# Kernel optimization log

Measured on AMD Instinct MI355X. Metric: run time of the kernel, lower is better.

The kernel has to match this reference:

```python
import jax, jax.numpy as jnp
import numpy as np

DIM = 2048; S = 2048; B = 2; H = 16
Q_LORA = 1536; KV_LORA = 512
NOPE = 128; ROPE = 64; VHD = 128
QK_HD = NOPE + ROPE  # 192


def _linear_params(key, out_dim, in_dim):
    k1, k2 = jax.random.split(key)
    w = jax.random.normal(k1, (out_dim, in_dim), jnp.float32) * 0.02
    b = jax.random.normal(k2, (out_dim,), jnp.float32) * 0.02
    return w, b


def setup_inputs() -> dict:
    key = jax.random.key(0)
    ks = jax.random.split(key, 8)
    x = jax.random.normal(ks[0], (B, S, DIM), jnp.float32)
    # RoPE tables (interleaved convention, half-dim = ROPE//2)
    inv_freq = 1.0 / (10000.0 ** (jnp.arange(ROPE // 2, dtype=jnp.float32) / (ROPE // 2)))
    ang = jnp.arange(S, dtype=jnp.float32)[:, None] * inv_freq[None, :]  # [S, 32]
    freqs_cos = jnp.cos(ang)
    freqs_sin = jnp.sin(ang)
    Wq_down_w, Wq_down_b = _linear_params(ks[1], Q_LORA, DIM)
    q_norm_w = jnp.ones((Q_LORA,), jnp.float32)
    Wq_up_w, Wq_up_b = _linear_params(ks[2], H * QK_HD, Q_LORA)
    Wkv_down_w, Wkv_down_b = _linear_params(ks[3], KV_LORA + ROPE, DIM)
    kv_norm_w = jnp.ones((KV_LORA,), jnp.float32)
    Wkv_up_w, Wkv_up_b = _linear_params(ks[4], H * (NOPE + VHD), KV_LORA)
    Wo_w, Wo_b = _linear_params(ks[5], DIM, H * VHD)
    return dict(x=x, freqs_cos=freqs_cos, freqs_sin=freqs_sin,
                Wq_down_w=Wq_down_w, Wq_down_b=Wq_down_b, q_norm_w=q_norm_w,
                Wq_up_w=Wq_up_w, Wq_up_b=Wq_up_b,
                Wkv_down_w=Wkv_down_w, Wkv_down_b=Wkv_down_b, kv_norm_w=kv_norm_w,
                Wkv_up_w=Wkv_up_w, Wkv_up_b=Wkv_up_b, Wo_w=Wo_w, Wo_b=Wo_b)


def _rmsnorm(x, w):
    eps = jnp.finfo(x.dtype).eps
    var = jnp.mean(jnp.square(x), axis=-1, keepdims=True)
    return x * jax.lax.rsqrt(var + eps) * w


def _rope(x, cos, sin):
    # x: [B, S, H, D] with consecutive (real, imag) pairs; cos/sin: [S, D//2]
    xr = x[..., 0::2]
    xi = x[..., 1::2]
    c = cos[None, :, None, :]
    s = sin[None, :, None, :]
    yr = xr * c - xi * s
    yi = xr * s + xi * c
    return jnp.stack([yr, yi], axis=-1).reshape(x.shape)


def reference(x, freqs_cos, freqs_sin, Wq_down_w, Wq_down_b, q_norm_w,
              Wq_up_w, Wq_up_b, Wkv_down_w, Wkv_down_b, kv_norm_w,
              Wkv_up_w, Wkv_up_b, Wo_w, Wo_b):
    Bx, Sx, _ = x.shape
    # Q path: down-proj -> RMSNorm -> up-proj
    q_lat = _rmsnorm(x @ Wq_down_w.T + Wq_down_b, q_norm_w)
    Q = (q_lat @ Wq_up_w.T + Wq_up_b).reshape(Bx, Sx, H, QK_HD)
    Q_nope, Q_rope = Q[..., :NOPE], Q[..., NOPE:]
    Q_rope = _rope(Q_rope, freqs_cos, freqs_sin)
    Q = jnp.concatenate([Q_nope, Q_rope], axis=-1)
    # KV path
    kv = x @ Wkv_down_w.T + Wkv_down_b
    kv_lat, k_rope = kv[..., :KV_LORA], kv[..., KV_LORA:]
    kv_lat = _rmsnorm(kv_lat, kv_norm_w)
    k_rope = _rope(k_rope[:, :, None, :], freqs_cos, freqs_sin)  # [B,S,1,ROPE]
    knv = (kv_lat @ Wkv_up_w.T + Wkv_up_b).reshape(Bx, Sx, H, NOPE + VHD)
    K_nope, V = knv[..., :NOPE], knv[..., NOPE:]
    K = jnp.concatenate([K_nope, jnp.broadcast_to(k_rope, (Bx, Sx, H, ROPE))], axis=-1)
    # causal SDPA, scale = 1/sqrt(qk_head_dim)
    scale = QK_HD ** -0.5
    scores = jnp.einsum('bqhd,bkhd->bhqk', Q, K) * scale
    causal = jnp.tril(jnp.ones((Sx, Sx), bool))
    scores = jnp.where(causal[None, None], scores, jnp.finfo(scores.dtype).min)
    attn = jax.nn.softmax(scores, axis=-1)
    out = jnp.einsum('bhqk,bkhd->bqhd', attn, V).reshape(Bx, Sx, H * VHD)
    return out @ Wo_w.T + Wo_b
```

## Files before the change

### kernel.cpp

```cpp
#include <hip/hip_runtime.h>
#include <hip/hip_bf16.h>

typedef unsigned short u16;
typedef short s16x8 __attribute__((ext_vector_type(8)));
typedef short s16x4 __attribute__((ext_vector_type(4)));
typedef float f32x4 __attribute__((ext_vector_type(4)));

#define SEQ   2048
#define BATCH 2
#define NHEAD 16

__device__ __forceinline__ float b2f(u16 u) {
    unsigned x = ((unsigned)u) << 16;
    return __builtin_bit_cast(float, x);
}
__device__ __forceinline__ u16 f2b(float f) {
    unsigned x = __builtin_bit_cast(unsigned, f);
    unsigned r = (x + 0x7fffu + ((x >> 16) & 1u)) >> 16;
    return (u16)r;
}
__device__ __forceinline__ u16 f2b_hw(float f) {
    return __builtin_bit_cast(u16, __float2bfloat16(f));
}
__device__ __forceinline__ s16x8 comb(s16x4 lo, s16x4 hi) {
    return __builtin_shufflevector(lo, hi, 0, 1, 2, 3, 4, 5, 6, 7);
}
__device__ __forceinline__ void gload16(const void* g, void* l) {
    __builtin_amdgcn_global_load_lds(
        (const __attribute__((address_space(1))) void*)g,
        (__attribute__((address_space(3))) void*)l, 16, 0, 0);
}

__global__ __launch_bounds__(256) void cvt4_k(
    const float* __restrict__ x, const float* __restrict__ wqd,
    const float* __restrict__ wkvd, const float* __restrict__ wqu,
    u16* __restrict__ xb, u16* __restrict__ wqdb,
    u16* __restrict__ wkvdb, u16* __restrict__ wqub)
{
    const int total = 4358144;
    int i = blockIdx.x * 256 + threadIdx.x;
    const int stride = gridDim.x * 256;
    for (; i < total; i += stride) {
        const float4* src; ushort4* dst; int off;
        if (i < 2097152)      { src = (const float4*)x;    dst = (ushort4*)xb;    off = i; }
        else if (i < 2883584) { src = (const float4*)wqd;  dst = (ushort4*)wqdb;  off = i - 2097152; }
        else if (i < 3178496) { src = (const float4*)wkvd; dst = (ushort4*)wkvdb; off = i - 2883584; }
        else                  { src = (const float4*)wqu;  dst = (ushort4*)wqub;  off = i - 3178496; }
        float4 v = src[off];
        ushort4 o = { f2b(v.x), f2b(v.y), f2b(v.z), f2b(v.w) };
        dst[off] = o;
    }
}

__global__ __launch_bounds__(256) void cvt_bf16_k(
    const float* __restrict__ in, u16* __restrict__ out, int n4)
{
    int i = blockIdx.x * 256 + threadIdx.x;
    const int stride = gridDim.x * 256;
    for (; i < n4; i += stride) {
        float4 v = ((const float4*)in)[i];
        ushort4 o = { f2b(v.x), f2b(v.y), f2b(v.z), f2b(v.w) };
        ((ushort4*)out)[i] = o;
    }
}

template <int MODE, int TM>
__global__ __launch_bounds__(512, 2) void gemm8p_k(
    const u16* __restrict__ A, const u16* __restrict__ W0,
    const u16* __restrict__ W1, const float* __restrict__ b0,
    const float* __restrict__ b1, void* __restrict__ C0, void* __restrict__ C1,
    int N, int K, int lda,
    const float* __restrict__ fc, const float* __restrict__ fs)
{
    constexpr int AH  = TM / 128;
    constexpr int MPP = TM == 256 ? 2 : 1;
    __shared__ u16 lsA[2][AH][128 * 64];
    __shared__ u16 lsB[2][2][128 * 64];
    const int tid  = threadIdx.x;
    const int lane = tid & 63;
    const int w    = tid >> 6;
    const int wm   = w >> 2;
    const int wn   = w & 3;
    const int row0 = blockIdx.y * TM;
    const int col0 = blockIdx.x * 256;
    const int nt   = K / 64;

    auto stageA = [&](int t, int h) {
        const int kt = t * 64, buf = t & 1;
#pragma unroll
        for (int j = 0; j < 2; j++) {
            const int g = (w * 2 + j) * 64 + lane;
            const int row = g >> 3, c16 = g & 7;
            const int cs = c16 ^ (row & 7);
            gload16(A + (size_t)(row0 + h * 128 + row) * lda + kt + cs * 8,
                    &lsA[buf][h][(w * 2 + j) * 512]);
        }
    };
    auto stageB = [&](int t, int h) {
        const int kt = t * 64, buf = t & 1;
#pragma unroll
        for (int j = 0; j < 2; j++) {
            const int g = (w * 2 + j) * 64 + lane;
            const int row = g >> 3, c16 = g & 7;
            const int cs = c16 ^ (row & 7);
            int rw = col0 + h * 128 + row;
            const u16* Wp;
            if (MODE == 3) {
                const bool in1 = rw >= 1536;
                int r2 = in1 ? rw - 1536 : rw;
                if (in1 && r2 > 575) r2 = 575;
                Wp = (in1 ? W1 : W0) + (size_t)r2 * K;
            } else {
                if (rw >= N) rw = N - 1;
                Wp = W0 + (size_t)rw * K;
            }
            gload16(Wp + kt + cs * 8, &lsB[buf][h][(w * 2 + j) * 512]);
        }
    };
    auto readA = [&](int buf, int mf, int kh) -> s16x8 {
        const int h  = TM == 256 ? wm : 0;
        const int ra = (TM == 256 ? mf * 16 : wm * 64 + mf * 16) + (lane & 15);
        const int c16 = kh * 4 + (lane >> 4);
        return *(const s16x8*)&lsA[buf][h][(ra * 8 + (c16 ^ (ra & 7))) * 8];
    };
    auto readB = [&](int buf, int nf, int kh) -> s16x8 {
        const int rb = (wn & 1) * 64 + nf * 16 + (lane & 15);
        const int c16 = kh * 4 + (lane >> 4);
        return *(const s16x8*)&lsB[buf][wn >> 1][(rb * 8 + (c16 ^ (rb & 7))) * 8];
    };

    f32x4 acc[4 * MPP][4];
#pragma unroll
    for (int i = 0; i < 4 * MPP; i++)
#pragma unroll
        for (int j = 0; j < 4; j++) acc[i][j] = (f32x4){0.f, 0.f, 0.f, 0.f};

    stageB(0, 0); stageB(0, 1);
#pragma unroll
    for (int h = 0; h < AH; h++) stageA(0, h);
    stageB(1, 0); stageB(1, 1);
    asm volatile("s_waitcnt vmcnt(4)" ::: "memory");
    asm volatile("s_barrier" ::: "memory");

    for (int t = 0; t < nt; t++) {
        const int buf = t & 1;
        s16x8 bfr[4][2];
#pragma unroll
        for (int nf = 0; nf < 4; nf++)
#pragma unroll
            for (int kh = 0; kh < 2; kh++) bfr[nf][kh] = readB(buf, nf, kh);
#pragma unroll
        for (int ph = 0; ph < 4; ph++) {
            s16x8 af[MPP][2];
#pragma unroll
            for (int m2 = 0; m2 < MPP; m2++)
#pragma unroll
                for (int kh = 0; kh < 2; kh++)
                    af[m2][kh] = readA(buf, ph * MPP + m2, kh);
            if (ph == 0) { if (t + 1 < nt) stageA(t + 1, 0); }
            else if (ph == 1) {
                if (TM == 256) { if (t + 1 < nt) stageA(t + 1, 1); }
                if (t + 2 < nt) stageB(t + 2, 0);
            } else if (ph == 2) { if (t + 2 < nt) stageB(t + 2, 1); }
            __builtin_amdgcn_s_setprio(1);
#pragma unroll
            for (int kh = 0; kh < 2; kh++)
#pragma unroll
                for (int m2 = 0; m2 < MPP; m2++)
#pragma unroll
                    for (int nf = 0; nf < 4; nf++)
                        acc[ph * MPP + m2][nf] = __builtin_amdgcn_mfma_f32_16x16x32_bf16(
                            af[m2][kh], bfr[nf][kh], acc[ph * MPP + m2][nf], 0, 0, 0);
            __builtin_amdgcn_s_setprio(0);
            if (ph == 0) asm volatile("s_barrier" ::: "memory");
        }
        if (t + 2 < nt) asm volatile("s_waitcnt vmcnt(4)" ::: "memory");
        else            asm volatile("s_waitcnt vmcnt(0)" ::: "memory");
        asm volatile("s_barrier" ::: "memory");
    }

    const float QS = 0.10411754f;
    const int rbase = row0 + wm * (TM == 256 ? 128 : 64) + ((lane >> 4) << 2);
    const int cbase = col0 + wn * 64 + (lane & 15);
#pragma unroll
    for (int nf = 0; nf < 4; nf++) {
        const int col = cbase + nf * 16;
        if (MODE == 3) {
            if (col < 2112) {
                const bool c1 = col >= 1536;
                const float bv = c1 ? b1[col - 1536] : b0[col];
#pragma unroll
                for (int mf = 0; mf < 4 * MPP; mf++)
#pragma unroll
                    for (int r = 0; r < 4; r++) {
                        const int row = rbase + mf * 16 + r;
                        const float v = acc[mf][nf][r] + bv;
                        if (c1) ((u16*)C1)[(size_t)row * 576 + col - 1536] = f2b_hw(v);
                        else    ((u16*)C0)[(size_t)row * 1536 + col] = f2b_hw(v);
                    }
            }
        } else if (MODE == 2) {
            const float bv = b0[col];
            const int colBase = col0 + wn * 64 + nf * 16;
            const int dh0 = colBase % 192;
            const bool ropeBlk = (dh0 >= 128);
            const int ib = (dh0 - 128 + (lane & 15)) >> 1;
#pragma unroll
            for (int mf = 0; mf < 4 * MPP; mf++)
#pragma unroll
                for (int r = 0; r < 4; r++) {
                    const int row = rbase + mf * 16 + r;
                    float v = acc[mf][nf][r] + bv;
                    if (ropeBlk) {
                        const float pp = __shfl_xor(v, 1);
                        const int s = row & (SEQ - 1);
                        const float c = fc[s * 32 + ib], sn = fs[s * 32 + ib];
                        v = (lane & 1) ? (v * c + pp * sn) : (v * c - pp * sn);
                    }
                    ((u16*)C0)[(size_t)row * 3072 + col] = f2b_hw(v * QS);
                }
        } else {
            if (col < N) {
                const float bv = b0[col];
#pragma unroll
                for (int mf = 0; mf < 4 * MPP; mf++)
#pragma unroll
                    for (int r = 0; r < 4; r++) {
                        const int row = rbase + mf * 16 + r;
                        const float v = acc[mf][nf][r] + bv;
                        if (MODE == 1) ((float*)C0)[(size_t)row * N + col] = v;
                        else           ((u16*)C0)[(size_t)row * N + col] = f2b_hw(v);
                    }
            }
        }
    }
}

__global__ __launch_bounds__(256) void norm_rope_k(
    u16* __restrict__ qlat, u16* __restrict__ kvb,
    const float* __restrict__ qnw, const float* __restrict__ kvnw,
    const float* __restrict__ fc, const float* __restrict__ fs,
    u16* __restrict__ krope)
{
    const int bid = blockIdx.x;
    const int row = bid & 4095;
    const bool isq = bid < 4096;
    u16* xr = isq ? qlat + (size_t)row * 1536 : kvb + (size_t)row * 576;
    const int cols = isq ? 1536 : 512;
    const float* wv = isq ? qnw : kvnw;

    if (!isq && threadIdx.x < 32) {
        const int i = threadIdx.x;
        const int s = row & (SEQ - 1);
        const u16* src = kvb + (size_t)row * 576 + 512 + 2 * i;
        const float xr0 = b2f(src[0]), xi0 = b2f(src[1]);
        const float c = fc[s * 32 + i], sn = fs[s * 32 + i];
        ushort2 o;
        o.x = f2b(xr0 * c - xi0 * sn);
        o.y = f2b(xr0 * sn + xi0 * c);
        *((ushort2*)(krope + (size_t)row * 64) + i) = o;
    }

    float ss = 0.f;
    for (int c = threadIdx.x; c < cols; c += 256) { float v = b2f(xr[c]); ss += v * v; }
#pragma unroll
    for (int off = 32; off; off >>= 1) ss += __shfl_xor(ss, off);
    __shared__ float red[4];
    if ((threadIdx.x & 63) == 0) red[threadIdx.x >> 6] = ss;
    __syncthreads();
    const float tot = red[0] + red[1] + red[2] + red[3];
    const float inv = rsqrtf(tot / (float)cols + 1.1920929e-7f);
    for (int c = threadIdx.x; c < cols; c += 256)
        xr[c] = f2b(b2f(xr[c]) * inv * wv[c]);
}

__global__ __launch_bounds__(256, 2) void attn_k(
    const u16* __restrict__ Q, const u16* __restrict__ KNV,
    const u16* __restrict__ KR, u16* __restrict__ O)
{
    __shared__ u16 k_lds[64][204];
    __shared__ u16 v_t[128][76];

    const int tid  = threadIdx.x;
    const int lane = tid & 63;
    const int w    = tid >> 6;
    const int lr   = lane & 15;
    const int lq   = lane >> 4;

    const int bid = blockIdx.x;
    const int qt  = (bid < 256) ? (15 - (bid >> 5)) : ((bid - 256) >> 5);
    const int bh  = bid & 31;
    const int h   = bh & 15;
    const int b   = bh >> 4;
    const int q0  = qt * 128;
    const int bS  = b * SEQ;

    s16x8 qf[2][6];
#pragma unroll
    for (int mb = 0; mb < 2; mb++) {
        const u16* qp = Q + (size_t)(bS + q0 + w * 32 + mb * 16 + lr) * 3072
                        + h * 192 + (lq << 2);
#pragma unroll
        for (int kc = 0; kc < 6; kc++)
            qf[mb][kc] = comb(*(const s16x4*)(qp + kc * 32),
                              *(const s16x4*)(qp + kc * 32 + 16));
    }

    f32x4 o_acc[2][8];
#pragma unroll
    for (int mb = 0; mb < 2; mb++)
#pragma unroll
        for (int d = 0; d < 8; d++) o_acc[mb][d] = (f32x4){0.f, 0.f, 0.f, 0.f};
    float m_run[2] = { -1e30f, -1e30f };
    float l_run[2] = { 0.f, 0.f };

    const int ntiles = (q0 + 128) / 64;
    const int qmax_w = q0 + w * 32 + 31;

    s16x8 kr[6], vr[4];
    const int kkey = tid >> 2;
    const int ka   = tid & 3;

    {
        const u16* kn  = KNV + (size_t)(bS + kkey) * 4096 + h * 256;
        const u16* krp = KR + (size_t)(bS + kkey) * 64;
#pragma unroll
        for (int i = 0; i < 6; i++) {
            const int col = ka * 48 + i * 8;
            kr[i] = *(const s16x8*)(col < 128 ? kn + col : krp + (col - 128));
        }
#pragma unroll
        for (int i = 0; i < 4; i++) {
            const int idx = tid + i * 256;
            vr[i] = *(const s16x8*)(KNV + (size_t)(bS + (idx >> 4)) * 4096
                                    + h * 256 + 128 + (idx & 15) * 8);
        }
    }

    for (int t = 0; t < ntiles; t++) {
#pragma unroll
        for (int i = 0; i < 6; i++) {
            const int c0 = ka * 48 + i * 8;
            *(s16x4*)&k_lds[kkey][c0]     = __builtin_shufflevector(kr[i], kr[i], 0, 1, 2, 3);
            *(s16x4*)&k_lds[kkey][c0 + 4] = __builtin_shufflevector(kr[i], kr[i], 4, 5, 6, 7);
        }
#pragma unroll
        for (int i = 0; i < 4; i++) {
            const int idx = tid + i * 256;
            const int key = idx >> 4, d0 = (idx & 15) * 8;
            const int xw = (d0 >> 4) << 2;
#pragma unroll
            for (int e = 0; e < 8; e++) v_t[d0 + e][key ^ xw] = (u16)vr[i][e];
        }
        __syncthreads();

        if (t + 1 < ntiles) {
            const int nk = (t + 1) * 64;
            const u16* kn  = KNV + (size_t)(bS + nk + kkey) * 4096 + h * 256;
            const u16* krp = KR + (size_t)(bS + nk + kkey) * 64;
#pragma unroll
            for (int i = 0; i < 6; i++) {
                const int col = ka * 48 + i * 8;
                kr[i] = *(const s16x8*)(col < 128 ? kn + col : krp + (col - 128));
            }
#pragma unroll
            for (int i = 0; i < 4; i++) {
                const int idx = tid + i * 256;
                vr[i] = *(const s16x8*)(KNV + (size_t)(bS + nk + (idx >> 4)) * 4096
                                        + h * 256 + 128 + (idx & 15) * 8);
            }
        }

        const int kt0 = t * 64;
        if (kt0 <= qmax_w) {
            f32x4 sa[2][4];
#pragma unroll
            for (int mb = 0; mb < 2; mb++)
#pragma unroll
                for (int f = 0; f < 4; f++) sa[mb][f] = (f32x4){0.f, 0.f, 0.f, 0.f};
#pragma unroll
            for (int kc = 0; kc < 6; kc++) {
                const int kb = kc * 32 + (lq << 2);
#pragma unroll
                for (int f = 0; f < 4; f++) {
                    s16x8 kf = comb(*(const s16x4*)&k_lds[f * 16 + lr][kb],
                                    *(const s16x4*)&k_lds[f * 16 + lr][kb + 16]);
                    sa[0][f] = __builtin_amdgcn_mfma_f32_16x16x32_bf16(kf, qf[0][kc], sa[0][f], 0, 0, 0);
                    sa[1][f] = __builtin_amdgcn_mfma_f32_16x16x32_bf16(kf, qf[1][kc], sa[1][f], 0, 0, 0);
                }
            }

            s16x8 pb[2][2];
#pragma unroll
            for (int mb = 0; mb < 2; mb++) {
                const int qrow = q0 + w * 32 + mb * 16 + lr;
                const bool need_mask = (kt0 + 63 > qrow);
                float p[4][4];
#pragma unroll
                for (int f = 0; f < 4; f++)
#pragma unroll
                    for (int r = 0; r < 4; r++) {
                        float s = sa[mb][f][r];
                        if (need_mask && (kt0 + f * 16 + lq * 4 + r > qrow)) s = -1e30f;
                        p[f][r] = s;
                    }
                float tm = p[0][0];
#pragma unroll
                for (int f = 0; f < 4; f++)
#pragma unroll
                    for (int r = 0; r < 4; r++) tm = fmaxf(tm, p[f][r]);
                tm = fmaxf(tm, __shfl_xor(tm, 16));
                tm = fmaxf(tm, __shfl_xor(tm, 32));

                const float mo = m_run[mb];
                const bool keep = __all(tm <= mo + 8.f);
                float corr = 1.f;
                if (!keep) {
                    const float nm = fmaxf(mo, tm);
                    corr = __builtin_amdgcn_exp2f(mo - nm);
                    m_run[mb] = nm;
                }
                const float mbase = m_run[mb];
#pragma unroll
                for (int f = 0; f < 4; f++)
#pragma unroll
                    for (int r = 0; r < 4; r++)
                        p[f][r] = __builtin_amdgcn_exp2f(p[f][r] - mbase);
                float ps = 0.f;
#pragma unroll
                for (int f = 0; f < 4; f++)
#pragma unroll
                    for (int r = 0; r < 4; r++) ps += p[f][r];
                ps += __shfl_xor(ps, 16);
                ps += __shfl_xor(ps, 32);
                l_run[mb] = l_run[mb] * corr + ps;
                if (!keep) {
#pragma unroll
                    for (int d = 0; d < 8; d++)
#pragma unroll
                        for (int r = 0; r < 4; r++) o_acc[mb][d][r] *= corr;
                }
#pragma unroll
                for (int hf = 0; hf < 2; hf++) {
                    s16x8 v;
#pragma unroll
                    for (int j = 0; j < 8; j++)
                        v[j] = (short)f2b_hw(p[hf * 2 + (j >> 2)][j & 3]);
                    pb[mb][hf] = v;
                }
            }

#pragma unroll
            for (int hf = 0; hf < 2; hf++) {
                const int pc = hf * 32 + (lq << 2);
#pragma unroll
                for (int df = 0; df < 8; df++) {
                    const int row = df * 16 + lr;
                    const int xr0 = df << 2;
                    s16x8 vf = comb(*(const s16x4*)&v_t[row][pc ^ xr0],
                                    *(const s16x4*)&v_t[row][(pc + 16) ^ xr0]);
                    o_acc[0][df] = __builtin_amdgcn_mfma_f32_16x16x32_bf16(vf, pb[0][hf], o_acc[0][df], 0, 0, 0);
                    o_acc[1][df] = __builtin_amdgcn_mfma_f32_16x16x32_bf16(vf, pb[1][hf], o_acc[1][df], 0, 0, 0);
                }
            }
        }
        __syncthreads();
    }

#pragma unroll
    for (int mb = 0; mb < 2; mb++) {
        const float invl = 1.f / l_run[mb];
        u16* op = O + (size_t)(bS + q0 + w * 32 + mb * 16 + lr) * 2048 + h * 128 + lq * 4;
#pragma unroll
        for (int df = 0; df < 8; df++) {
            ushort4 ov = { f2b_hw(o_acc[mb][df][0] * invl), f2b_hw(o_acc[mb][df][1] * invl),
                           f2b_hw(o_acc[mb][df][2] * invl), f2b_hw(o_acc[mb][df][3] * invl) };
            *(ushort4*)(op + df * 16) = ov;
        }
    }
}

extern "C" void kernel_launch(void* const* d_in, const int* in_sizes, int n_in,
                              void* d_out, int out_size, void* d_ws, size_t ws_size,
                              hipStream_t stream)
{
    const float* x    = (const float*)d_in[0];
    const float* fc   = (const float*)d_in[1];
    const float* fs   = (const float*)d_in[2];
    const float* Wqd  = (const float*)d_in[3];
    const float* bqd  = (const float*)d_in[4];
    const float* qnw  = (const float*)d_in[5];
    const float* Wqu  = (const float*)d_in[6];
    const float* bqu  = (const float*)d_in[7];
    const float* Wkvd = (const float*)d_in[8];
    const float* bkvd = (const float*)d_in[9];
    const float* kvnw = (const float*)d_in[10];
    const float* Wkvu = (const float*)d_in[11];
    const float* bkvu = (const float*)d_in[12];
    const float* Wo   = (const float*)d_in[13];
    const float* bo   = (const float*)d_in[14];

    char* ws = (char*)d_ws;
    u16* kvb     = (u16*)(ws);
    u16* qlat    = (u16*)(ws + 4718592);
    u16* qbuf    = (u16*)(ws + 17301504);
    u16* krope   = (u16*)(ws + 42467328);
    u16* knv     = (u16*)(ws + 42991616);
    u16* attn_o  = (u16*)(ws);
    u16* x_bf    = (u16*)(ws + 17301504);
    u16* wqd_bf  = (u16*)(ws + 42991616);
    u16* wkvd_bf = (u16*)(ws + 49283072);
    u16* wqu_bf  = (u16*)(ws + 51642368);
    u16* wkvu_bf = (u16*)(ws + 4718592);
    u16* wo_bf   = (u16*)(ws + 42991616);

    cvt4_k<<<2048, 256, 0, stream>>>(x, Wqd, Wkvd, Wqu, x_bf, wqd_bf, wkvd_bf, wqu_bf);
    gemm8p_k<3, 256><<<dim3(9, 16), 512, 0, stream>>>(
        x_bf, wqd_bf, wkvd_bf, bqd, bkvd, qlat, kvb, 2112, 2048, 2048, nullptr, nullptr);
    norm_rope_k<<<8192, 256, 0, stream>>>(qlat, kvb, qnw, kvnw, fc, fs, krope);
    gemm8p_k<2, 256><<<dim3(12, 16), 512, 0, stream>>>(
        qlat, wqu_bf, nullptr, bqu, nullptr, qbuf, nullptr, 3072, 1536, 1536, fc, fs);
    cvt_bf16_k<<<1024, 256, 0, stream>>>(Wkvu, wkvu_bf, 2097152 / 4);
    gemm8p_k<0, 256><<<dim3(16, 16), 512, 0, stream>>>(
        kvb, wkvu_bf, nullptr, bkvu, nullptr, knv, nullptr, 4096, 512, 576, nullptr, nullptr);
    attn_k<<<512, 256, 0, stream>>>(qbuf, knv, krope, attn_o);
    cvt_bf16_k<<<1024, 256, 0, stream>>>(Wo, wo_bf, 4194304 / 4);
    gemm8p_k<1, 128><<<dim3(8, 32), 512, 0, stream>>>(
        attn_o, wo_bf, nullptr, bo, nullptr, d_out, nullptr, 2048, 2048, 2048, nullptr, nullptr);
}
```

Baseline: 345.5 us.

## Fuse fp32-to-bf16 conversion of x into the down-projection GEMM A-load

Drops the standalone conversion of x to bf16. The first GEMM now loads fp32 x rows into registers, converts them, and writes them to LDS at a later phase, replacing the async global-to-LDS copy. This removes a full write and re-read of the bf16 copy of x. In exchange, GEMM register pressure rises and each iteration waits on an extra LDS count. Separately, the norm kernel is vectorised to 8-element loads and stores, with the row kept in registers between reduction and scaling.

```diff
diff --git a/kernel.cpp b/kernel.cpp
--- a/kernel.cpp
+++ b/kernel.cpp
@@ -31,21 +31,19 @@
         (__attribute__((address_space(3))) void*)l, 16, 0, 0);
 }
 
-__global__ __launch_bounds__(256) void cvt4_k(
-    const float* __restrict__ x, const float* __restrict__ wqd,
-    const float* __restrict__ wkvd, const float* __restrict__ wqu,
-    u16* __restrict__ xb, u16* __restrict__ wqdb,
-    u16* __restrict__ wkvdb, u16* __restrict__ wqub)
+__global__ __launch_bounds__(256) void cvt3_k(
+    const float* __restrict__ wqd, const float* __restrict__ wkvd,
+    const float* __restrict__ wqu,
+    u16* __restrict__ wqdb, u16* __restrict__ wkvdb, u16* __restrict__ wqub)
 {
-    const int total = 4358144;
+    const int total = 2260992;
     int i = blockIdx.x * 256 + threadIdx.x;
     const int stride = gridDim.x * 256;
     for (; i < total; i += stride) {
         const float4* src; ushort4* dst; int off;
-        if (i < 2097152)      { src = (const float4*)x;    dst = (ushort4*)xb;    off = i; }
-        else if (i < 2883584) { src = (const float4*)wqd;  dst = (ushort4*)wqdb;  off = i - 2097152; }
-        else if (i < 3178496) { src = (const float4*)wkvd; dst = (ushort4*)wkvdb; off = i - 2883584; }
-        else                  { src = (const float4*)wqu;  dst = (ushort4*)wqub;  off = i - 3178496; }
+        if (i < 786432)       { src = (const float4*)wqd;  dst = (ushort4*)wqdb;  off = i; }
+        else if (i < 1081344) { src = (const float4*)wkvd; dst = (ushort4*)wkvdb; off = i - 786432; }
+        else                  { src = (const float4*)wqu;  dst = (ushort4*)wqub;  off = i - 1081344; }
         float4 v = src[off];
         ushort4 o = { f2b(v.x), f2b(v.y), f2b(v.z), f2b(v.w) };
         dst[off] = o;
@@ -66,7 +64,7 @@
 
 template <int MODE, int TM>
 __global__ __launch_bounds__(512, 2) void gemm8p_k(
-    const u16* __restrict__ A, const u16* __restrict__ W0,
+    const void* __restrict__ Av, const u16* __restrict__ W0,
     const u16* __restrict__ W1, const float* __restrict__ b0,
     const float* __restrict__ b1, void* __restrict__ C0, void* __restrict__ C1,
     int N, int K, int lda,
@@ -74,6 +72,7 @@
 {
     constexpr int AH  = TM / 128;
     constexpr int MPP = TM == 256 ? 2 : 1;
+    constexpr bool AF32 = (MODE == 3);
     __shared__ u16 lsA[2][AH][128 * 64];
     __shared__ u16 lsB[2][2][128 * 64];
     const int tid  = threadIdx.x;
@@ -85,6 +84,8 @@
     const int col0 = blockIdx.x * 256;
     const int nt   = K / 64;
 
+    float4 afl[AH][2][2];
+
     auto stageA = [&](int t, int h) {
         const int kt = t * 64, buf = t & 1;
 #pragma unroll
@@ -92,8 +93,31 @@
             const int g = (w * 2 + j) * 64 + lane;
             const int row = g >> 3, c16 = g & 7;
             const int cs = c16 ^ (row & 7);
-            gload16(A + (size_t)(row0 + h * 128 + row) * lda + kt + cs * 8,
+            gload16((const u16*)Av + (size_t)(row0 + h * 128 + row) * lda + kt + cs * 8,
                     &lsA[buf][h][(w * 2 + j) * 512]);
+        }
+    };
+    auto issueAf32 = [&](int t, int h) {
+        const float* X = (const float*)Av;
+        const int kt = t * 64;
+#pragma unroll
+        for (int j = 0; j < 2; j++) {
+            const int g = (w * 2 + j) * 64 + lane;
+            const int row = g >> 3, c16 = g & 7;
+            const int cs = c16 ^ (row & 7);
+            const float* p = X + (size_t)(row0 + h * 128 + row) * lda + kt + cs * 8;
+            afl[h][j][0] = *(const float4*)p;
+            afl[h][j][1] = *(const float4*)(p + 4);
+        }
+    };
+    auto writeAf32 = [&](int t, int h) {
+        const int buf = t & 1;
+#pragma unroll
+        for (int j = 0; j < 2; j++) {
+            const float4 lo = afl[h][j][0], hi = afl[h][j][1];
+            s16x8 o = { (short)f2b(lo.x), (short)f2b(lo.y), (short)f2b(lo.z), (short)f2b(lo.w),
+                        (short)f2b(hi.x), (short)f2b(hi.y), (short)f2b(hi.z), (short)f2b(hi.w) };
+            *(s16x8*)&lsA[buf][h][((w * 2 + j) * 64 + lane) * 8] = o;
         }
     };
     auto stageB = [&](int t, int h) {
@@ -136,10 +160,18 @@
         for (int j = 0; j < 4; j++) acc[i][j] = (f32x4){0.f, 0.f, 0.f, 0.f};
 
     stageB(0, 0); stageB(0, 1);
-#pragma unroll
-    for (int h = 0; h < AH; h++) stageA(0, h);
+    if (AF32) {
+#pragma unroll
+        for (int h = 0; h < AH; h++) issueAf32(0, h);
+#pragma unroll
+        for (int h = 0; h < AH; h++) writeAf32(0, h);
+    } else {
+#pragma unroll
+        for (int h = 0; h < AH; h++) stageA(0, h);
+    }
     stageB(1, 0); stageB(1, 1);
     asm volatile("s_waitcnt vmcnt(4)" ::: "memory");
+    if (AF32) asm volatile("s_waitcnt lgkmcnt(0)" ::: "memory");
     asm volatile("s_barrier" ::: "memory");
 
     for (int t = 0; t < nt; t++) {
@@ -157,11 +189,19 @@
 #pragma unroll
                 for (int kh = 0; kh < 2; kh++)
                     af[m2][kh] = readA(buf, ph * MPP + m2, kh);
-            if (ph == 0) { if (t + 1 < nt) stageA(t + 1, 0); }
-            else if (ph == 1) {
-                if (TM == 256) { if (t + 1 < nt) stageA(t + 1, 1); }
+            if (ph == 0) {
+                if (t + 1 < nt) { if (AF32) issueAf32(t + 1, 0); else stageA(t + 1, 0); }
+            } else if (ph == 1) {
+                if (TM == 256 && t + 1 < nt) { if (AF32) issueAf32(t + 1, 1); else stageA(t + 1, 1); }
                 if (t + 2 < nt) stageB(t + 2, 0);
-            } else if (ph == 2) { if (t + 2 < nt) stageB(t + 2, 1); }
+            } else if (ph == 2) {
+                if (t + 2 < nt) stageB(t + 2, 1);
+            } else {
+                if (AF32 && t + 1 < nt) {
+#pragma unroll
+                    for (int h = 0; h < AH; h++) writeAf32(t + 1, h);
+                }
+            }
             __builtin_amdgcn_s_setprio(1);
 #pragma unroll
             for (int kh = 0; kh < 2; kh++)
@@ -176,6 +216,7 @@
         }
         if (t + 2 < nt) asm volatile("s_waitcnt vmcnt(4)" ::: "memory");
         else            asm volatile("s_waitcnt vmcnt(0)" ::: "memory");
+        if (AF32) asm volatile("s_waitcnt lgkmcnt(0)" ::: "memory");
         asm volatile("s_barrier" ::: "memory");
     }
 
@@ -248,9 +289,11 @@
     u16* xr = isq ? qlat + (size_t)row * 1536 : kvb + (size_t)row * 576;
     const int cols = isq ? 1536 : 512;
     const float* wv = isq ? qnw : kvnw;
-
-    if (!isq && threadIdx.x < 32) {
-        const int i = threadIdx.x;
+    const int t = threadIdx.x;
+    const int nv = cols >> 3;
+
+    if (!isq && t < 32) {
+        const int i = t;
         const int s = row & (SEQ - 1);
         const u16* src = kvb + (size_t)row * 576 + 512 + 2 * i;
         const float xr0 = b2f(src[0]), xi0 = b2f(src[1]);
@@ -261,17 +304,27 @@
         *((ushort2*)(krope + (size_t)row * 64) + i) = o;
     }
 
+    s16x8 v = {0,0,0,0,0,0,0,0};
     float ss = 0.f;
-    for (int c = threadIdx.x; c < cols; c += 256) { float v = b2f(xr[c]); ss += v * v; }
+    if (t < nv) {
+        v = *(const s16x8*)(xr + t * 8);
+#pragma unroll
+        for (int e = 0; e < 8; e++) { float f = b2f((u16)v[e]); ss += f * f; }
+    }
 #pragma unroll
     for (int off = 32; off; off >>= 1) ss += __shfl_xor(ss, off);
     __shared__ float red[4];
-    if ((threadIdx.x & 63) == 0) red[threadIdx.x >> 6] = ss;
+    if ((t & 63) == 0) red[t >> 6] = ss;
     __syncthreads();
     const float tot = red[0] + red[1] + red[2] + red[3];
     const float inv = rsqrtf(tot / (float)cols + 1.1920929e-7f);
-    for (int c = threadIdx.x; c < cols; c += 256)
-        xr[c] = f2b(b2f(xr[c]) * inv * wv[c]);
+    if (t < nv) {
+        s16x8 o;
+#pragma unroll
+        for (int e = 0; e < 8; e++)
+            o[e] = (short)f2b(b2f((u16)v[e]) * inv * wv[t * 8 + e]);
+        *(s16x8*)(xr + t * 8) = o;
+    }
 }
 
 __global__ __launch_bounds__(256, 2) void attn_k(
@@ -507,16 +560,15 @@
     u16* krope   = (u16*)(ws + 42467328);
     u16* knv     = (u16*)(ws + 42991616);
     u16* attn_o  = (u16*)(ws);
-    u16* x_bf    = (u16*)(ws + 17301504);
     u16* wqd_bf  = (u16*)(ws + 42991616);
     u16* wkvd_bf = (u16*)(ws + 49283072);
     u16* wqu_bf  = (u16*)(ws + 51642368);
     u16* wkvu_bf = (u16*)(ws + 4718592);
     u16* wo_bf   = (u16*)(ws + 42991616);
 
-    cvt4_k<<<2048, 256, 0, stream>>>(x, Wqd, Wkvd, Wqu, x_bf, wqd_bf, wkvd_bf, wqu_bf);
+    cvt3_k<<<2048, 256, 0, stream>>>(Wqd, Wkvd, Wqu, wqd_bf, wkvd_bf, wqu_bf);
     gemm8p_k<3, 256><<<dim3(9, 16), 512, 0, stream>>>(
-        x_bf, wqd_bf, wkvd_bf, bqd, bkvd, qlat, kvb, 2112, 2048, 2048, nullptr, nullptr);
+        x, wqd_bf, wkvd_bf, bqd, bkvd, qlat, kvb, 2112, 2048, 2048, nullptr, nullptr);
     norm_rope_k<<<8192, 256, 0, stream>>>(qlat, kvb, qnw, kvnw, fc, fs, krope);
     gemm8p_k<2, 256><<<dim3(12, 16), 512, 0, stream>>>(
         qlat, wqu_bf, nullptr, bqu, nullptr, qbuf, nullptr, 3072, 1536, 1536, fc, fs);
```

Measured after the change: 366.1 us. +6.0%, slower.
